# Kernel optimization log

Measured on AMD Instinct MI355X. Metric: run time of the kernel, lower is better.

The kernel has to match this reference:

```python
import jax, jax.numpy as jnp
import numpy as np

B, S, D, H = 4, 2048, 1024, 16
HD = D // H  # head dim = 64


def setup_inputs() -> dict:
    key = jax.random.key(0)
    ks = jax.random.split(key, 6)
    scale = D ** -0.5
    x = jax.random.normal(ks[0], (B, S, D), dtype=jnp.float32)
    # per-head q/k/v projections stacked: [H, D, HD] (bias-free, as in GPT Head)
    Wq = jax.random.normal(ks[1], (H, D, HD), dtype=jnp.float32) * scale
    Wk = jax.random.normal(ks[2], (H, D, HD), dtype=jnp.float32) * scale
    Wv = jax.random.normal(ks[3], (H, D, HD), dtype=jnp.float32) * scale
    # output projection Linear(D, D) with bias
    Wp = jax.random.normal(ks[4], (D, D), dtype=jnp.float32) * scale
    bp = jax.random.normal(ks[5], (D,), dtype=jnp.float32) * 0.01
    return {"x": x, "Wq": Wq, "Wk": Wk, "Wv": Wv, "Wp": Wp, "bp": bp}


def reference(x, Wq, Wk, Wv, Wp, bp):
    # q,k,v: [B, H, S, HD]
    q = jnp.einsum("bsd,hdk->bhsk", x, Wq)
    k = jnp.einsum("bsd,hdk->bhsk", x, Wk)
    v = jnp.einsum("bsd,hdk->bhsk", x, Wv)
    scale = HD ** -0.5
    # attention scores [B, H, S, S] with causal mask
    scores = jnp.einsum("bhsk,bhtk->bhst", q, k) * scale
    causal = jnp.tril(jnp.ones((S, S), dtype=bool))
    scores = jnp.where(causal, scores, jnp.finfo(scores.dtype).min)
    att = jax.nn.softmax(scores, axis=-1)
    out = jnp.einsum("bhst,bhtk->bhsk", att, v)  # [B, H, S, HD]
    # concat heads -> [B, S, D], then output projection
    out = out.transpose(0, 2, 1, 3).reshape(B, S, D)
    return out @ Wp + bp
```

## Files before the change

### kernel.cpp

```cpp
#include <hip/hip_runtime.h>
#include <stdint.h>

#define B_  4
#define S_  2048
#define D_  1024
#define H_  16
#define HD_ 64

typedef __attribute__((ext_vector_type(8))) short bf16x8;
typedef __attribute__((ext_vector_type(4))) short bf16x4;
typedef __attribute__((ext_vector_type(4))) float f32x4;

#define MFMA32(a, b, c) __builtin_amdgcn_mfma_f32_16x16x32_bf16(a, b, c, 0, 0, 0)

__device__ __forceinline__ unsigned short f2bf(float f) {
  union { float f; uint32_t u; } cv; cv.f = f;
  uint32_t x = cv.u;
  uint32_t r = (x + 0x7fffu + ((x >> 16) & 1u)) >> 16;
  return (unsigned short)r;
}

__device__ __forceinline__ float fexp2(float x) {
#if __has_builtin(__builtin_amdgcn_exp2f)
  return __builtin_amdgcn_exp2f(x);
#else
  return exp2f(x);
#endif
}

__device__ __forceinline__ uint32_t pk2(float lo, float hi) {
  union { float f; uint32_t u; } a, b;
  a.f = lo; b.f = hi;
#if __has_builtin(__builtin_amdgcn_perm)
  return __builtin_amdgcn_perm(b.u, a.u, 0x07060302u);
#else
  return (b.u & 0xffff0000u) | (a.u >> 16);
#endif
}

__device__ __forceinline__ void gload_lds16(const unsigned short* g, unsigned short* l) {
  __builtin_amdgcn_global_load_lds((const __attribute__((address_space(1))) void*)g,
                                   (__attribute__((address_space(3))) void*)l, 16, 0, 0);
}

__global__ void k_cast_x(const float* __restrict__ x, unsigned short* __restrict__ xb) {
  size_t i = ((size_t)blockIdx.x * 256 + threadIdx.x) * 8;
  float4 a = *(const float4*)(x + i);
  float4 b = *(const float4*)(x + i + 4);
  bf16x8 o;
  o[0] = (short)f2bf(a.x); o[1] = (short)f2bf(a.y);
  o[2] = (short)f2bf(a.z); o[3] = (short)f2bf(a.w);
  o[4] = (short)f2bf(b.x); o[5] = (short)f2bf(b.y);
  o[6] = (short)f2bf(b.z); o[7] = (short)f2bf(b.w);
  *(bf16x8*)(xb + i) = o;
}

__global__ void k_wqkv_t(const float* __restrict__ Wq, const float* __restrict__ Wk,
                         const float* __restrict__ Wv, unsigned short* __restrict__ W1T) {
  __shared__ unsigned short tile[64][65];
  const float* W = (blockIdx.z == 0) ? Wq : (blockIdx.z == 1) ? Wk : Wv;
  int h = blockIdx.y;
  int d0 = blockIdx.x * 64;
  int tx = threadIdx.x & 63;
  int tg = threadIdx.x >> 6;
  const float* src = W + (size_t)h * (D_ * HD_) + (size_t)d0 * HD_;
#pragma unroll
  for (int r = 0; r < 16; ++r) {
    int dy = tg * 16 + r;
    tile[tx][dy] = f2bf(src[(size_t)dy * HD_ + tx]);
  }
  __syncthreads();
  unsigned short* dst = W1T + ((size_t)blockIdx.z * 1024 + (size_t)h * 64) * 1024 + d0;
#pragma unroll
  for (int r = 0; r < 16; ++r) {
    int hd = tg * 16 + r;
    dst[(size_t)hd * 1024 + tx] = tile[hd][tx];
  }
}

__global__ void k_wp_t(const float* __restrict__ Wp, unsigned short* __restrict__ WpT) {
  __shared__ unsigned short tile[64][65];
  int n0 = blockIdx.x * 64, k0 = blockIdx.y * 64;
  int tx = threadIdx.x & 63;
  int tg = threadIdx.x >> 6;
#pragma unroll
  for (int r = 0; r < 16; ++r) {
    int ky = tg * 16 + r;
    tile[tx][ky] = f2bf(Wp[(size_t)(k0 + ky) * D_ + n0 + tx]);
  }
  __syncthreads();
#pragma unroll
  for (int r = 0; r < 16; ++r) {
    int ny = tg * 16 + r;
    WpT[(size_t)(n0 + ny) * D_ + k0 + tx] = tile[ny][tx];
  }
}

__device__ __forceinline__ void stage_half(const unsigned short* g0, unsigned short* l0, int tid) {
  int r0 = tid >> 2, s0 = tid & 3;
  gload_lds16(g0 + (size_t)r0 * 1024 + ((s0 ^ ((r0 >> 1) & 3)) << 3), l0 + tid * 8);
  int r1 = r0 + 128;
  gload_lds16(g0 + (size_t)r1 * 1024 + ((s0 ^ ((r1 >> 1) & 3)) << 3), l0 + 4096 + tid * 8);
}

__device__ __forceinline__ bf16x8 rd_swz(const unsigned short* base, int row, int g) {
  return *(const bf16x8*)&base[row * 32 + ((g ^ ((row >> 1) & 3)) << 3)];
}

__global__ __launch_bounds__(512, 2) void k_gemm_qk(const unsigned short* __restrict__ xb,
                                                    const unsigned short* __restrict__ W1T,
                                                    unsigned short* __restrict__ qb,
                                                    unsigned short* __restrict__ kb) {
  __shared__ __align__(16) unsigned short As[32768];
  __shared__ __align__(16) unsigned short Bs[32768];
  int tid = threadIdx.x;
  int lane = tid & 63;
  int wid = tid >> 6;
  int c = lane & 15, g = lane >> 4;
  int wr = wid >> 2, wc = wid & 3;
  int bid = blockIdx.x;
  int xcd = bid & 7, idx = bid >> 3;
  int by = (xcd << 2) | (idx & 3);
  int bx = idx >> 2;
  int m0 = by << 8, n0 = bx << 8;
  const unsigned short* gA = xb + (size_t)m0 * 1024;
  const unsigned short* gB = W1T + (size_t)n0 * 1024;

  f32x4 acc[8][4];
#pragma unroll
  for (int i = 0; i < 8; ++i)
#pragma unroll
    for (int n = 0; n < 4; ++n) acc[i][n] = (f32x4){0.f, 0.f, 0.f, 0.f};

  stage_half(gA + 0,  As + 0, tid);
  stage_half(gB + 0,  Bs + 0, tid);
  stage_half(gA + 32, As + 8192, tid);
  stage_half(gB + 32, Bs + 8192, tid);

  for (int t = 0; t < 16; ++t) {
    int sl = (t & 1) << 14;
    int so = sl ^ 16384;
    int kn = (t + 1) << 6;
    bool pf = (t < 15);
    const unsigned short* Asl = As + sl;
    const unsigned short* Bsl = Bs + sl;
    bf16x8 bf[4];

    asm volatile("s_waitcnt vmcnt(4)" ::: "memory");
    __builtin_amdgcn_s_barrier();
    if (pf) stage_half(gA + kn, As + so, tid);
#pragma unroll
    for (int n = 0; n < 4; ++n) bf[n] = rd_swz(Bsl, wc * 64 + n * 16 + c, g);
    {
      bf16x8 af[4];
#pragma unroll
      for (int j = 0; j < 4; ++j) af[j] = rd_swz(Asl, wr * 128 + j * 16 + c, g);
      __builtin_amdgcn_s_setprio(1);
#pragma unroll
      for (int j = 0; j < 4; ++j)
#pragma unroll
        for (int n = 0; n < 4; ++n) acc[j][n] = MFMA32(af[j], bf[n], acc[j][n]);
      __builtin_amdgcn_s_setprio(0);
    }
    if (pf) stage_half(gB + kn, Bs + so, tid);
    {
      bf16x8 af[4];
#pragma unroll
      for (int j = 0; j < 4; ++j) af[j] = rd_swz(Asl, wr * 128 + (4 + j) * 16 + c, g);
      __builtin_amdgcn_s_setprio(1);
#pragma unroll
      for (int j = 0; j < 4; ++j)
#pragma unroll
        for (int n = 0; n < 4; ++n) acc[4 + j][n] = MFMA32(af[j], bf[n], acc[4 + j][n]);
      __builtin_amdgcn_s_setprio(0);
    }
    if (pf) asm volatile("s_waitcnt vmcnt(4)" ::: "memory");
    else    asm volatile("s_waitcnt vmcnt(0)" ::: "memory");
    __builtin_amdgcn_s_barrier();
    if (pf) stage_half(gA + kn + 32, As + so + 8192, tid);
#pragma unroll
    for (int n = 0; n < 4; ++n) bf[n] = rd_swz(Bsl + 8192, wc * 64 + n * 16 + c, g);
    {
      bf16x8 af[4];
#pragma unroll
      for (int j = 0; j < 4; ++j) af[j] = rd_swz(Asl + 8192, wr * 128 + j * 16 + c, g);
      __builtin_amdgcn_s_setprio(1);
#pragma unroll
      for (int j = 0; j < 4; ++j)
#pragma unroll
        for (int n = 0; n < 4; ++n) acc[j][n] = MFMA32(af[j], bf[n], acc[j][n]);
      __builtin_amdgcn_s_setprio(0);
    }
    if (pf) stage_half(gB + kn + 32, Bs + so + 8192, tid);
    {
      bf16x8 af[4];
#pragma unroll
      for (int j = 0; j < 4; ++j) af[j] = rd_swz(Asl + 8192, wr * 128 + (4 + j) * 16 + c, g);
      __builtin_amdgcn_s_setprio(1);
#pragma unroll
      for (int j = 0; j < 4; ++j)
#pragma unroll
        for (int n = 0; n < 4; ++n) acc[4 + j][n] = MFMA32(af[j], bf[n], acc[4 + j][n]);
      __builtin_amdgcn_s_setprio(0);
    }
  }

  int Cnb = n0 + wc * 64;
  int qkv = Cnb >> 10;
  int h = (Cnb >> 6) & 15;
  int b = m0 >> 11;
  int s0 = m0 & 2047;
  unsigned short* dst = ((qkv == 0) ? qb : kb) + ((size_t)(b * 16 + h) * S_) * HD_;
  float sc = (qkv == 0) ? 0.18033688011112042f : 1.0f;
#pragma unroll
  for (int mrep = 0; mrep < 8; ++mrep)
#pragma unroll
    for (int n = 0; n < 4; ++n)
#pragma unroll
      for (int r = 0; r < 4; ++r) {
        int s = s0 + wr * 128 + mrep * 16 + 4 * g + r;
        int hd = n * 16 + c;
        dst[(size_t)s * HD_ + hd] = f2bf(acc[mrep][n][r] * sc);
      }
}

__global__ __launch_bounds__(256) void k_gemm_vt(const unsigned short* __restrict__ W1T,
                                                 const unsigned short* __restrict__ xb,
                                                 unsigned short* __restrict__ vt) {
  __shared__ __align__(16) unsigned short As[128 * 32];
  __shared__ __align__(16) unsigned short Bs[128 * 32];
  const int K = 1024;
  int tid = threadIdx.x;
  int lane = tid & 63;
  int w = tid >> 6;
  int c = lane & 15, g = lane >> 4;
  int wr = w >> 1, wc = w & 1;
  int nwg = gridDim.x * gridDim.y;
  int bid = blockIdx.y * gridDim.x + blockIdx.x;
  int swzb = (bid & 7) * (nwg >> 3) + (bid >> 3);
  int bx = swzb % gridDim.x, by = swzb / gridDim.x;
  int m0 = by * 128;
  int n0 = bx * 128;
  const unsigned short* Av = W1T + (size_t)2048 * 1024;
  f32x4 acc[4][4];
#pragma unroll
  for (int m = 0; m < 4; ++m)
#pragma unroll
    for (int n = 0; n < 4; ++n) acc[m][n] = (f32x4){0.f, 0.f, 0.f, 0.f};

  int t0 = tid, t1 = tid + 256;
  const unsigned short* ga0 = Av + (size_t)(m0 + (t0 >> 2)) * K + 8 * (t0 & 3);
  const unsigned short* ga1 = Av + (size_t)(m0 + (t1 >> 2)) * K + 8 * (t1 & 3);
  const unsigned short* gb0 = xb + (size_t)(n0 + (t0 >> 2)) * K + 8 * (t0 & 3);
  const unsigned short* gb1 = xb + (size_t)(n0 + (t1 >> 2)) * K + 8 * (t1 & 3);

  for (int kk = 0; kk < K; kk += 32) {
    __syncthreads();
    gload_lds16(ga0 + kk, &As[t0 * 8]);
    gload_lds16(ga1 + kk, &As[t1 * 8]);
    gload_lds16(gb0 + kk, &Bs[t0 * 8]);
    gload_lds16(gb1 + kk, &Bs[t1 * 8]);
    __syncthreads();
    bf16x8 af[4], bfr[4];
#pragma unroll
    for (int m = 0; m < 4; ++m)
      af[m] = *(const bf16x8*)&As[(wr * 64 + m * 16 + c) * 32 + 8 * g];
#pragma unroll
    for (int n = 0; n < 4; ++n)
      bfr[n] = *(const bf16x8*)&Bs[(wc * 64 + n * 16 + c) * 32 + 8 * g];
#pragma unroll
    for (int m = 0; m < 4; ++m)
#pragma unroll
      for (int n = 0; n < 4; ++n) acc[m][n] = MFMA32(af[m], bfr[n], acc[m][n]);
  }

  int b = (n0 >> 11);
#pragma unroll
  for (int m = 0; m < 4; ++m)
#pragma unroll
    for (int n = 0; n < 4; ++n)
#pragma unroll
      for (int r = 0; r < 4; ++r) {
        int vm = m0 + wr * 64 + m * 16 + 4 * g + r;
        int Cn = n0 + wc * 64 + n * 16 + c;
        int s = Cn & 2047;
        vt[((size_t)(b << 10) + vm) * S_ + s] = f2bf(acc[m][n][r]);
      }
}

__device__ __forceinline__ void stage_kv(const unsigned short* kp, const unsigned short* vp,
                                         int tb, unsigned short* Ks, unsigned short* Vs,
                                         int tid) {
  int i0 = tid, i1 = tid + 256;
  int r0 = i0 >> 3, ch0 = ((i0 & 7) ^ (r0 & 7)) << 3;
  int r1 = i1 >> 3, ch1 = ((i1 & 7) ^ (r1 & 7)) << 3;
  gload_lds16(kp + (size_t)(tb + r0) * HD_ + ch0, &Ks[i0 * 8]);
  gload_lds16(kp + (size_t)(tb + r1) * HD_ + ch1, &Ks[i1 * 8]);
  gload_lds16(vp + (size_t)r0 * S_ + tb + ch0, &Vs[i0 * 8]);
  gload_lds16(vp + (size_t)r1 * S_ + tb + ch1, &Vs[i1 * 8]);
}

__global__ __launch_bounds__(256) void k_attn(const unsigned short* __restrict__ qb,
                                              const unsigned short* __restrict__ kb,
                                              const unsigned short* __restrict__ vt,
                                              unsigned short* __restrict__ attn) {
  __shared__ __align__(16) unsigned short Ks[2][64 * 64];
  __shared__ __align__(16) unsigned short Vs[2][64 * 64];
  int tid = threadIdx.x;
  int lane = tid & 63;
  int w = tid >> 6;
  int c = lane & 15, g = lane >> 4;
  int bid = blockIdx.x;
  int xcd = bid & 7, idx = bid >> 3;
  int bh = (xcd << 3) | (idx & 7);
  int j = 15 - (idx >> 3);
  const unsigned short* kp = kb + (size_t)bh * S_ * HD_;
  const unsigned short* vp = vt + (size_t)bh * HD_ * S_;
  int b = bh >> 4, h = bh & 15;

  int koff[4][2], voff[4][2][2];
#pragma unroll
  for (int k4 = 0; k4 < 4; ++k4) {
    int row = k4 * 16 + c, rx = row & 7;
    koff[k4][0] = row * 64 + ((g ^ rx) << 3);
    koff[k4][1] = row * 64 + (((4 + g) ^ rx) << 3);
  }
#pragma unroll
  for (int c4 = 0; c4 < 4; ++c4) {
    int row = c4 * 16 + c, rx = row & 7;
#pragma unroll
    for (int ks = 0; ks < 2; ++ks) {
      int e0 = ks * 32 + 4 * g;
      int e1 = e0 + 16;
      voff[c4][ks][0] = row * 64 + ((((e0 >> 3) ^ rx) << 3) | (e0 & 7));
      voff[c4][ks][1] = row * 64 + ((((e1 >> 3) ^ rx) << 3) | (e1 & 7));
    }
  }

  int q0w = j * 128 + w * 32;
  const unsigned short* qp = qb + ((size_t)bh * S_ + q0w) * HD_;
  bf16x8 qf[2][2];
#pragma unroll
  for (int qs = 0; qs < 2; ++qs)
#pragma unroll
    for (int h2 = 0; h2 < 2; ++h2)
      qf[qs][h2] = *(const bf16x8*)(qp + (size_t)(qs * 16 + c) * HD_ + h2 * 32 + 8 * g);

  const f32x4 fz = {0.f, 0.f, 0.f, 0.f};
  f32x4 oacc[4][2];
#pragma unroll
  for (int c4 = 0; c4 < 4; ++c4)
#pragma unroll
    for (int qs = 0; qs < 2; ++qs) oacc[c4][qs] = fz;
  float m[2] = {-1e30f, -1e30f};
  float l[2] = {0.f, 0.f};

  int nkb = 2 * j + 2;
  int nkw = (q0w + 95) >> 6;

  stage_kv(kp, vp, 0, Ks[0], Vs[0], tid);
  __syncthreads();

  for (int kt = 0; kt < nkb; ++kt) {
    int cur = kt & 1;
    if (kt + 1 < nkb) stage_kv(kp, vp, (kt + 1) << 6, Ks[cur ^ 1], Vs[cur ^ 1], tid);
    if (kt < nkw) {
      int tb = kt << 6;
      const unsigned short* KsC = Ks[cur];
      const unsigned short* VsC = Vs[cur];
      f32x4 st[4][2];
#pragma unroll
      for (int k4 = 0; k4 < 4; ++k4) {
        bf16x8 a0 = *(const bf16x8*)&KsC[koff[k4][0]];
        bf16x8 a1 = *(const bf16x8*)&KsC[koff[k4][1]];
#pragma unroll
        for (int qs = 0; qs < 2; ++qs) {
          f32x4 t0 = MFMA32(a0, qf[qs][0], fz);
          st[k4][qs] = MFMA32(a1, qf[qs][1], t0);
        }
      }
      if (tb + 63 > q0w) {
#pragma unroll
        for (int k4 = 0; k4 < 4; ++k4)
#pragma unroll
          for (int qs = 0; qs < 2; ++qs)
#pragma unroll
            for (int r = 0; r < 4; ++r)
              if (tb + k4 * 16 + 4 * g + r > q0w + qs * 16 + c) st[k4][qs][r] = -1e30f;
      }
      bf16x8 pa[2][2];
#pragma unroll
      for (int qs = 0; qs < 2; ++qs) {
        float mx = -1e30f;
#pragma unroll
        for (int k4 = 0; k4 < 4; ++k4)
#pragma unroll
          for (int r = 0; r < 4; ++r) mx = fmaxf(mx, st[k4][qs][r]);
        mx = fmaxf(mx, __shfl_xor(mx, 16));
        mx = fmaxf(mx, __shfl_xor(mx, 32));
        if (!__all(mx - m[qs] <= 8.f)) {
          float m_new = fmaxf(m[qs], mx);
          float resc = fexp2(m[qs] - m_new);
          m[qs] = m_new;
          float rb0 = __shfl(resc, 4 * g + 0);
          float rb1 = __shfl(resc, 4 * g + 1);
          float rb2 = __shfl(resc, 4 * g + 2);
          float rb3 = __shfl(resc, 4 * g + 3);
#pragma unroll
          for (int c4 = 0; c4 < 4; ++c4) {
            oacc[c4][qs][0] *= rb0; oacc[c4][qs][1] *= rb1;
            oacc[c4][qs][2] *= rb2; oacc[c4][qs][3] *= rb3;
          }
          l[qs] *= resc;
        }
        float mh = m[qs];
        float rs = 0.f;
#pragma unroll
        for (int k4 = 0; k4 < 4; ++k4)
#pragma unroll
          for (int r = 0; r < 4; ++r) {
            float e = fexp2(st[k4][qs][r] - mh);
            st[k4][qs][r] = e;
            rs += e;
          }
        l[qs] += rs;
#pragma unroll
        for (int ks = 0; ks < 2; ++ks) {
          union { uint32_t wd[4]; bf16x8 v; } pu;
          int ks2 = ks * 2;
          pu.wd[0] = pk2(st[ks2][qs][0], st[ks2][qs][1]);
          pu.wd[1] = pk2(st[ks2][qs][2], st[ks2][qs][3]);
          pu.wd[2] = pk2(st[ks2 + 1][qs][0], st[ks2 + 1][qs][1]);
          pu.wd[3] = pk2(st[ks2 + 1][qs][2], st[ks2 + 1][qs][3]);
          pa[qs][ks] = pu.v;
        }
      }
#pragma unroll
      for (int c4 = 0; c4 < 4; ++c4) {
#pragma unroll
        for (int ks = 0; ks < 2; ++ks) {
          bf16x4 v0 = *(const bf16x4*)&VsC[voff[c4][ks][0]];
          bf16x4 v1 = *(const bf16x4*)&VsC[voff[c4][ks][1]];
          bf16x8 vf;
          vf[0] = v0[0]; vf[1] = v0[1]; vf[2] = v0[2]; vf[3] = v0[3];
          vf[4] = v1[0]; vf[5] = v1[1]; vf[6] = v1[2]; vf[7] = v1[3];
#pragma unroll
          for (int qs = 0; qs < 2; ++qs)
            oacc[c4][qs] = MFMA32(pa[qs][ks], vf, oacc[c4][qs]);
        }
      }
    }
    __syncthreads();
  }
#pragma unroll
  for (int qs = 0; qs < 2; ++qs) {
    float lt = l[qs];
    lt += __shfl_xor(lt, 16);
    lt += __shfl_xor(lt, 32);
    float linv = 1.f / lt;
    float lb0 = __shfl(linv, 4 * g + 0);
    float lb1 = __shfl(linv, 4 * g + 1);
    float lb2 = __shfl(linv, 4 * g + 2);
    float lb3 = __shfl(linv, 4 * g + 3);
    float lb[4] = {lb0, lb1, lb2, lb3};
    unsigned short* op = attn + ((size_t)b * S_ + q0w + qs * 16) * D_ + h * HD_;
#pragma unroll
    for (int c4 = 0; c4 < 4; ++c4)
#pragma unroll
      for (int r = 0; r < 4; ++r)
        op[(size_t)(4 * g + r) * D_ + c4 * 16 + c] = f2bf(oacc[c4][qs][r] * lb[r]);
  }
}

__global__ __launch_bounds__(256) void k_gemm_out(const unsigned short* __restrict__ at,
                                                  const unsigned short* __restrict__ WpT,
                                                  const float* __restrict__ bp,
                                                  float* __restrict__ out) {
  __shared__ __align__(16) unsigned short As[128 * 32];
  __shared__ __align__(16) unsigned short Bs[128 * 32];
  const int K = 1024;
  int tid = threadIdx.x;
  int lane = tid & 63;
  int w = tid >> 6;
  int c = lane & 15, g = lane >> 4;
  int wr = w >> 1, wc = w & 1;
  int nwg = gridDim.x * gridDim.y;
  int bid = blockIdx.y * gridDim.x + blockIdx.x;
  int swzb = (bid & 7) * (nwg >> 3) + (bid >> 3);
  int bx = swzb % gridDim.x, by = swzb / gridDim.x;
  int m0 = by * 128;
  int n0 = bx * 128;
  f32x4 acc[4][4];
#pragma unroll
  for (int m = 0; m < 4; ++m)
#pragma unroll
    for (int n = 0; n < 4; ++n) acc[m][n] = (f32x4){0.f, 0.f, 0.f, 0.f};

  int t0 = tid, t1 = tid + 256;
  const unsigned short* ga0 = at + (size_t)(m0 + (t0 >> 2)) * K + 8 * (t0 & 3);
  const unsigned short* ga1 = at + (size_t)(m0 + (t1 >> 2)) * K + 8 * (t1 & 3);
  const unsigned short* gb0 = WpT + (size_t)(n0 + (t0 >> 2)) * K + 8 * (t0 & 3);
  const unsigned short* gb1 = WpT + (size_t)(n0 + (t1 >> 2)) * K + 8 * (t1 & 3);

  for (int kk = 0; kk < K; kk += 32) {
    __syncthreads();
    gload_lds16(ga0 + kk, &As[t0 * 8]);
    gload_lds16(ga1 + kk, &As[t1 * 8]);
    gload_lds16(gb0 + kk, &Bs[t0 * 8]);
    gload_lds16(gb1 + kk, &Bs[t1 * 8]);
    __syncthreads();
    bf16x8 af[4], bfr[4];
#pragma unroll
    for (int m = 0; m < 4; ++m)
      af[m] = *(const bf16x8*)&As[(wr * 64 + m * 16 + c) * 32 + 8 * g];
#pragma unroll
    for (int n = 0; n < 4; ++n)
      bfr[n] = *(const bf16x8*)&Bs[(wc * 64 + n * 16 + c) * 32 + 8 * g];
#pragma unroll
    for (int m = 0; m < 4; ++m)
#pragma unroll
      for (int n = 0; n < 4; ++n) acc[m][n] = MFMA32(af[m], bfr[n], acc[m][n]);
  }

#pragma unroll
  for (int m = 0; m < 4; ++m)
#pragma unroll
    for (int n = 0; n < 4; ++n)
#pragma unroll
      for (int r = 0; r < 4; ++r) {
        int R = m0 + wr * 64 + m * 16 + 4 * g + r;
        int Cn = n0 + wc * 64 + n * 16 + c;
        out[(size_t)R * D_ + Cn] = acc[m][n][r] + bp[Cn];
      }
}

extern "C" void kernel_launch(void* const* d_in, const int* in_sizes, int n_in,
                              void* d_out, int out_size, void* d_ws, size_t ws_size,
                              hipStream_t stream) {
  const float* x  = (const float*)d_in[0];
  const float* Wq = (const float*)d_in[1];
  const float* Wk = (const float*)d_in[2];
  const float* Wv = (const float*)d_in[3];
  const float* Wp = (const float*)d_in[4];
  const float* bp = (const float*)d_in[5];
  float* out = (float*)d_out;
  char* ws = (char*)d_ws;
  unsigned short* xb  = (unsigned short*)(ws);
  unsigned short* w1t = (unsigned short*)(ws + (size_t)(16u << 20));
  unsigned short* wpt = (unsigned short*)(ws + (size_t)(22u << 20));
  unsigned short* qb  = (unsigned short*)(ws + (size_t)(24u << 20));
  unsigned short* kb  = (unsigned short*)(ws + (size_t)(40u << 20));
  unsigned short* vt  = (unsigned short*)(ws + (size_t)(56u << 20));
  unsigned short* at  = xb;

  k_cast_x<<<dim3(4096), dim3(256), 0, stream>>>(x, xb);
  k_wqkv_t<<<dim3(16, 16, 3), dim3(256), 0, stream>>>(Wq, Wk, Wv, w1t);
  k_wp_t<<<dim3(16, 16), dim3(256), 0, stream>>>(Wp, wpt);
  k_gemm_qk<<<dim3(256), dim3(512), 0, stream>>>(xb, w1t, qb, kb);
  k_gemm_vt<<<dim3(64, 8), dim3(256), 0, stream>>>(w1t, xb, vt);
  k_attn<<<dim3(1024), dim3(256), 0, stream>>>(qb, kb, vt, at);
  k_gemm_out<<<dim3(8, 64), dim3(256), 0, stream>>>(at, wpt, bp, out);
}
```

Before: 177.3 us.

## Double query rows per attention block to raise K/V reuse

Each wave of the attention kernel now handles 64 query rows instead of 32, so a block covers 256 queries and the grid halves to 512 blocks. Each K/V tile staged in LDS and the K fragments loaded into registers now feed twice as many MFMAs, and the causal mask is applied only on the diagonal tile, which now lines up exactly with each wave's 64-row slice. The cost is more registers per wave (accumulators and Q fragments double), which may lower occupancy, and fewer blocks for load balancing across the causal triangle.

```diff
diff --git a/kernel.cpp b/kernel.cpp
--- a/kernel.cpp
+++ b/kernel.cpp
@@ -313,7 +313,7 @@
   int bid = blockIdx.x;
   int xcd = bid & 7, idx = bid >> 3;
   int bh = (xcd << 3) | (idx & 7);
-  int j = 15 - (idx >> 3);
+  int j = 7 - (idx >> 3);
   const unsigned short* kp = kb + (size_t)bh * S_ * HD_;
   const unsigned short* vp = vt + (size_t)bh * HD_ * S_;
   int b = bh >> 4, h = bh & 15;
@@ -337,26 +337,26 @@
     }
   }
 
-  int q0w = j * 128 + w * 32;
+  int q0w = j * 256 + w * 64;
   const unsigned short* qp = qb + ((size_t)bh * S_ + q0w) * HD_;
-  bf16x8 qf[2][2];
-#pragma unroll
-  for (int qs = 0; qs < 2; ++qs)
+  bf16x8 qf[4][2];
+#pragma unroll
+  for (int qs = 0; qs < 4; ++qs)
 #pragma unroll
     for (int h2 = 0; h2 < 2; ++h2)
       qf[qs][h2] = *(const bf16x8*)(qp + (size_t)(qs * 16 + c) * HD_ + h2 * 32 + 8 * g);
 
   const f32x4 fz = {0.f, 0.f, 0.f, 0.f};
-  f32x4 oacc[4][2];
+  f32x4 oacc[4][4];
 #pragma unroll
   for (int c4 = 0; c4 < 4; ++c4)
 #pragma unroll
-    for (int qs = 0; qs < 2; ++qs) oacc[c4][qs] = fz;
-  float m[2] = {-1e30f, -1e30f};
-  float l[2] = {0.f, 0.f};
-
-  int nkb = 2 * j + 2;
-  int nkw = (q0w + 95) >> 6;
+    for (int qs = 0; qs < 4; ++qs) oacc[c4][qs] = fz;
+  float m[4] = {-1e30f, -1e30f, -1e30f, -1e30f};
+  float l[4] = {0.f, 0.f, 0.f, 0.f};
+
+  int nkb = 4 * j + 4;
+  int nkw = (q0w >> 6) + 1;
 
   stage_kv(kp, vp, 0, Ks[0], Vs[0], tid);
   __syncthreads();
@@ -368,34 +368,35 @@
       int tb = kt << 6;
       const unsigned short* KsC = Ks[cur];
       const unsigned short* VsC = Vs[cur];
-      f32x4 st[4][2];
+      bool diag = (tb == q0w);
+      bf16x8 kf[4][2];
 #pragma unroll
       for (int k4 = 0; k4 < 4; ++k4) {
-        bf16x8 a0 = *(const bf16x8*)&KsC[koff[k4][0]];
-        bf16x8 a1 = *(const bf16x8*)&KsC[koff[k4][1]];
-#pragma unroll
-        for (int qs = 0; qs < 2; ++qs) {
-          f32x4 t0 = MFMA32(a0, qf[qs][0], fz);
-          st[k4][qs] = MFMA32(a1, qf[qs][1], t0);
+        kf[k4][0] = *(const bf16x8*)&KsC[koff[k4][0]];
+        kf[k4][1] = *(const bf16x8*)&KsC[koff[k4][1]];
+      }
+      bf16x8 pa[4][2];
+#pragma unroll
+      for (int qs = 0; qs < 4; ++qs) {
+        f32x4 st[4];
+#pragma unroll
+        for (int k4 = 0; k4 < 4; ++k4) {
+          f32x4 t0 = MFMA32(kf[k4][0], qf[qs][0], fz);
+          st[k4] = MFMA32(kf[k4][1], qf[qs][1], t0);
         }
-      }
-      if (tb + 63 > q0w) {
+        if (diag) {
+          int qrow = q0w + qs * 16 + c;
+#pragma unroll
+          for (int k4 = 0; k4 < 4; ++k4)
+#pragma unroll
+            for (int r = 0; r < 4; ++r)
+              if (tb + k4 * 16 + 4 * g + r > qrow) st[k4][r] = -1e30f;
+        }
+        float mx = -1e30f;
 #pragma unroll
         for (int k4 = 0; k4 < 4; ++k4)
 #pragma unroll
-          for (int qs = 0; qs < 2; ++qs)
-#pragma unroll
-            for (int r = 0; r < 4; ++r)
-              if (tb + k4 * 16 + 4 * g + r > q0w + qs * 16 + c) st[k4][qs][r] = -1e30f;
-      }
-      bf16x8 pa[2][2];
-#pragma unroll
-      for (int qs = 0; qs < 2; ++qs) {
-        float mx = -1e30f;
-#pragma unroll
-        for (int k4 = 0; k4 < 4; ++k4)
-#pragma unroll
-          for (int r = 0; r < 4; ++r) mx = fmaxf(mx, st[k4][qs][r]);
+          for (int r = 0; r < 4; ++r) mx = fmaxf(mx, st[k4][r]);
         mx = fmaxf(mx, __shfl_xor(mx, 16));
         mx = fmaxf(mx, __shfl_xor(mx, 32));
         if (!__all(mx - m[qs] <= 8.f)) {
@@ -419,8 +420,8 @@
         for (int k4 = 0; k4 < 4; ++k4)
 #pragma unroll
           for (int r = 0; r < 4; ++r) {
-            float e = fexp2(st[k4][qs][r] - mh);
-            st[k4][qs][r] = e;
+            float e = fexp2(st[k4][r] - mh);
+            st[k4][r] = e;
             rs += e;
           }
         l[qs] += rs;
@@ -428,10 +429,10 @@
         for (int ks = 0; ks < 2; ++ks) {
           union { uint32_t wd[4]; bf16x8 v; } pu;
           int ks2 = ks * 2;
-          pu.wd[0] = pk2(st[ks2][qs][0], st[ks2][qs][1]);
-          pu.wd[1] = pk2(st[ks2][qs][2], st[ks2][qs][3]);
-          pu.wd[2] = pk2(st[ks2 + 1][qs][0], st[ks2 + 1][qs][1]);
-          pu.wd[3] = pk2(st[ks2 + 1][qs][2], st[ks2 + 1][qs][3]);
+          pu.wd[0] = pk2(st[ks2][0], st[ks2][1]);
+          pu.wd[1] = pk2(st[ks2][2], st[ks2][3]);
+          pu.wd[2] = pk2(st[ks2 + 1][0], st[ks2 + 1][1]);
+          pu.wd[3] = pk2(st[ks2 + 1][2], st[ks2 + 1][3]);
           pa[qs][ks] = pu.v;
         }
       }
@@ -445,7 +446,7 @@
           vf[0] = v0[0]; vf[1] = v0[1]; vf[2] = v0[2]; vf[3] = v0[3];
           vf[4] = v1[0]; vf[5] = v1[1]; vf[6] = v1[2]; vf[7] = v1[3];
 #pragma unroll
-          for (int qs = 0; qs < 2; ++qs)
+          for (int qs = 0; qs < 4; ++qs)
             oacc[c4][qs] = MFMA32(pa[qs][ks], vf, oacc[c4][qs]);
         }
       }
@@ -453,7 +454,7 @@
     __syncthreads();
   }
 #pragma unroll
-  for (int qs = 0; qs < 2; ++qs) {
+  for (int qs = 0; qs < 4; ++qs) {
     float lt = l[qs];
     lt += __shfl_xor(lt, 16);
     lt += __shfl_xor(lt, 32);
@@ -558,6 +559,6 @@
   k_wp_t<<<dim3(16, 16), dim3(256), 0, stream>>>(Wp, wpt);
   k_gemm_qk<<<dim3(256), dim3(512), 0, stream>>>(xb, w1t, qb, kb);
   k_gemm_vt<<<dim3(64, 8), dim3(256), 0, stream>>>(w1t, xb, vt);
-  k_attn<<<dim3(1024), dim3(256), 0, stream>>>(qb, kb, vt, at);
+  k_attn<<<dim3(512), dim3(256), 0, stream>>>(qb, kb, vt, at);
   k_gemm_out<<<dim3(8, 64), dim3(256), 0, stream>>>(at, wpt, bp, out);
 }
```

New measurement: 204.8 us. 1.16x slower.
